# Performance work log

Hardware: AMD Instinct MI355X
Metric: run time of the kernel (lower is better)

The kernel has to match this reference:

```python
import jax, jax.numpy as jnp
import numpy as np

N_NODES = 100000
N_EDGES = 1600000


def setup_inputs() -> dict:
    key = jax.random.key(0)
    k1, k2, k3, k4 = jax.random.split(key, 4)
    x = jax.random.normal(k1, (N_NODES, 16), dtype=jnp.float32)
    edge_index = jax.random.randint(k2, (2, N_EDGES), 0, N_NODES, dtype=jnp.int32)
    # Glorot-ish init for the two GCN layers
    W1 = jax.random.normal(k3, (16, 32), dtype=jnp.float32) * (1.0 / np.sqrt(16))
    b1 = jnp.zeros((32,), dtype=jnp.float32)
    W2 = jax.random.normal(k4, (32, 2), dtype=jnp.float32) * (1.0 / np.sqrt(32))
    b2 = jnp.zeros((2,), dtype=jnp.float32)
    return {"x": x, "edge_index": edge_index, "W1": W1, "b1": b1, "W2": W2, "b2": b2}


def _gcn_conv(x, W, b, src, dst, norm, n_nodes):
    # PyG GCNConv: h = X @ W; aggregate norm * h[src] at dst; add bias.
    h = x @ W                                   # [N, out]
    msg = h[src] * norm[:, None]                # [E+N, out] gather + scale
    out = jax.ops.segment_sum(msg, dst, num_segments=n_nodes)
    return out + b


def reference(x, edge_index, W1, b1, W2, b2):
    n = x.shape[0]
    self_loops = jnp.arange(n, dtype=edge_index.dtype)
    src = jnp.concatenate([edge_index[0], self_loops])  # [E+N]
    dst = jnp.concatenate([edge_index[1], self_loops])
    # Symmetric GCN normalization: deg computed on graph with self-loops
    deg = jax.ops.segment_sum(jnp.ones_like(dst, dtype=x.dtype), dst, num_segments=n)
    dis = jnp.where(deg > 0, jax.lax.rsqrt(deg), 0.0)   # deg^{-1/2}
    norm = dis[src] * dis[dst]                          # [E+N]

    h = jax.nn.relu(_gcn_conv(x, W1, b1, src, dst, norm, n))
    out = _gcn_conv(h, W2, b2, src, dst, norm, n)
    return out
```

## Files before the change

kernel.cpp:

```cpp
#include <hip/hip_runtime.h>
#include <hip/hip_fp16.h>

static constexpr int N  = 100000;
static constexpr int E  = 1600000;
static constexpr int B  = 256;

static constexpr int BC     = 1024;
static constexpr int NBLKC  = 256;
static constexpr int CHUNKC = E / NBLKC;
static constexpr int PERC   = (CHUNKC + BC - 1) / BC;
static constexpr int NBUCK  = (N + 127) / 128;
static constexpr int SLAB   = 3072;
static constexpr int GCS    = 16;


__global__ __launch_bounds__(BC) void kC_scatter(
        const int* __restrict__ src, const int* __restrict__ dst,
        int* __restrict__ gcur, int* __restrict__ gslab) {
    __shared__ int lhist[NBUCK];
    __shared__ int lbase[NBUCK];
    __shared__ int gb[NBUCK];
    __shared__ int wsum[16];
    __shared__ int stage[CHUNKC];

    int t = threadIdx.x, blk = blockIdx.x;
    for (int i = t; i < NBUCK; i += BC) lhist[i] = 0;
    __syncthreads();

    int eb = blk * CHUNKC;
    int ds[PERC], ss[PERC];
#pragma unroll
    for (int k = 0; k < PERC; ++k) {
        int idx = k * BC + t;
        if (idx < CHUNKC) {
            ds[k] = dst[eb + idx];
            ss[k] = src[eb + idx];
            atomicAdd(&lhist[ds[k] >> 7], 1);
        }
    }
    __syncthreads();

    int lane = t & 63, wv = t >> 6;
    int val = (t < NBUCK) ? lhist[t] : 0;
    int inc = val;
#pragma unroll
    for (int off = 1; off < 64; off <<= 1) {
        int u = __shfl_up(inc, off, 64);
        if (lane >= off) inc += u;
    }
    if (lane == 63) wsum[wv] = inc;
    __syncthreads();
    if (wv == 0) {
        int wval = (lane < 16) ? wsum[lane] : 0;
        int winc = wval;
#pragma unroll
        for (int off = 1; off < 16; off <<= 1) {
            int u = __shfl_up(winc, off, 64);
            if (lane >= off) winc += u;
        }
        if (lane < 16) wsum[lane] = winc - wval;
    }
    __syncthreads();
    if (t < NBUCK) lbase[t] = wsum[wv] + inc - val;
    __syncthreads();

    if (t < NBUCK) {
        int h = lhist[t];
        if (h > 0) gb[t] = t * SLAB + atomicAdd(&gcur[t * GCS], h);
        lhist[t] = 0;
    }
    __syncthreads();

#pragma unroll
    for (int k = 0; k < PERC; ++k) {
        int idx = k * BC + t;
        if (idx < CHUNKC) {
            int d = ds[k], b = d >> 7;
            int r = atomicAdd(&lhist[b], 1);
            stage[lbase[b] + r] = ss[k] | ((d & 127) << 17);
        }
    }
    __syncthreads();

    if (t < NBUCK) {
        int len = lhist[t];
        if (len > 0) {
            int s0 = lbase[t];
            int g  = gb[t];
            int cap = (t + 1) * SLAB - g;
            if (cap < 0) cap = 0;
            if (len > cap) len = cap;
            for (int i = 0; i < len; ++i) gslab[g + i] = stage[s0 + i];
        }
    }
}


__global__ void kD1_deg(const int* __restrict__ gcur, const int* __restrict__ gslab,
                        int* __restrict__ rofs, const float4* __restrict__ x4,
                        __half* __restrict__ xpre) {
    __shared__ int c[128];
    __shared__ int wq[2];
    int t = threadIdx.x, b = blockIdx.x;
    if (t < 128) c[t] = 0;
    __syncthreads();

    int ne = min(gcur[b * GCS], SLAB);
    int base = b * SLAB;
    int ne4 = ne & ~3;
    for (int k = 4 * t; k < ne4; k += 4 * B) {
        int4 p4 = *(const int4*)(gslab + base + k);
        atomicAdd(&c[p4.x >> 17], 1);
        atomicAdd(&c[p4.y >> 17], 1);
        atomicAdd(&c[p4.z >> 17], 1);
        atomicAdd(&c[p4.w >> 17], 1);
    }
    if (t < ne - ne4) atomicAdd(&c[gslab[base + ne4 + t] >> 17], 1);
    __syncthreads();

    int lane = t & 63, wv = t >> 6;
    int val = (t < 128) ? c[t] : 0;
    int inc = val;
#pragma unroll
    for (int off = 1; off < 64; off <<= 1) {
        int u = __shfl_up(inc, off, 64);
        if (lane >= off) inc += u;
    }
    if (t == 63) wq[0] = inc;
    __syncthreads();
    if (t < 128) rofs[b * 129 + t] = base + inc - val + ((wv == 1) ? wq[0] : 0);
    if (t == 128) rofs[b * 129 + 128] = base + ne;

    int n = b * 128 + (t >> 1), h = t & 1;
    if (n < N) {
        float d = rsqrtf((float)(c[t >> 1] + 1));
        float4 u0 = x4[(size_t)n * 4 + h * 2];
        float4 u1 = x4[(size_t)n * 4 + h * 2 + 1];
        ushort4 p0, p1;
        p0.x = __half_as_ushort(__float2half(u0.x * d));
        p0.y = __half_as_ushort(__float2half(u0.y * d));
        p0.z = __half_as_ushort(__float2half(u0.z * d));
        p0.w = __half_as_ushort(__float2half(u0.w * d));
        p1.x = __half_as_ushort(__float2half(u1.x * d));
        p1.y = __half_as_ushort(__float2half(u1.y * d));
        p1.z = __half_as_ushort(__float2half(u1.z * d));
        p1.w = __half_as_ushort(__float2half(u1.w * d));
        *(ushort4*)(xpre + (size_t)n * 16 + h * 8)     = p0;
        *(ushort4*)(xpre + (size_t)n * 16 + h * 8 + 4) = p1;
    }
}


__global__ __launch_bounds__(B) void kD2_agg(
        const __half* __restrict__ xpre, const int* __restrict__ gslab,
        const int* __restrict__ rofs, const float* __restrict__ W1,
        const float* __restrict__ b1, const float* __restrict__ W2,
        float2* __restrict__ hpre) {
    __shared__ int st1[SLAB];
    __shared__ int cur[128];
    __shared__ int lofs[129];
    __shared__ float acc[128 * 17];
    __shared__ float sW1[512], sb1[32], sW2[64];
    int t = threadIdx.x, b = blockIdx.x;
    for (int i = t; i < 512; i += B) sW1[i] = W1[i];
    if (t < 32) sb1[t] = b1[t];
    if (t < 64) sW2[t] = W2[t];
    if (t < 128) cur[t] = 0;
    int base = b * SLAB;
    if (t < 129) lofs[t] = rofs[b * 129 + t] - base;
    __syncthreads();

    int ne = lofs[128];
    for (int k = t; k < ne; k += B) {
        int p = gslab[base + k];
        int lo = p >> 17;
        int r = atomicAdd(&cur[lo], 1);
        st1[lofs[lo] + r] = p & 0x1FFFF;
    }
    __syncthreads();

    int nl = t >> 1, h = t & 1;
    int n = b * 128 + nl;
    if (n < N) {
        int rs = lofs[nl], re = lofs[nl + 1];
        float a0, a1, a2, a3, a4, a5, a6, a7;
        {
            int4 w = *(const int4*)(xpre + (size_t)n * 16 + h * 8);
            float2 q0 = __half22float2(*(__half2*)&w.x);
            float2 q1 = __half22float2(*(__half2*)&w.y);
            float2 q2 = __half22float2(*(__half2*)&w.z);
            float2 q3 = __half22float2(*(__half2*)&w.w);
            a0 = q0.x; a1 = q0.y; a2 = q1.x; a3 = q1.y;
            a4 = q2.x; a5 = q2.y; a6 = q3.x; a7 = q3.y;
        }
        auto add8 = [&](int4 w) {
            float2 q0 = __half22float2(*(__half2*)&w.x);
            float2 q1 = __half22float2(*(__half2*)&w.y);
            float2 q2 = __half22float2(*(__half2*)&w.z);
            float2 q3 = __half22float2(*(__half2*)&w.w);
            a0 += q0.x; a1 += q0.y; a2 += q1.x; a3 += q1.y;
            a4 += q2.x; a5 += q2.y; a6 += q3.x; a7 += q3.y;
        };
        int k = rs;
        for (; k + 4 <= re; k += 4) {
            int s0 = st1[k], s1 = st1[k + 1], s2 = st1[k + 2], s3 = st1[k + 3];
            int4 v0 = *(const int4*)(xpre + (size_t)s0 * 16 + h * 8);
            int4 v1 = *(const int4*)(xpre + (size_t)s1 * 16 + h * 8);
            int4 v2 = *(const int4*)(xpre + (size_t)s2 * 16 + h * 8);
            int4 v3 = *(const int4*)(xpre + (size_t)s3 * 16 + h * 8);
            add8(v0); add8(v1); add8(v2); add8(v3);
        }
        for (; k < re; ++k)
            add8(*(const int4*)(xpre + (size_t)st1[k] * 16 + h * 8));
        float* row = acc + nl * 17 + h * 8;
        row[0] = a0; row[1] = a1; row[2] = a2; row[3] = a3;
        row[4] = a4; row[5] = a5; row[6] = a6; row[7] = a7;
    }
    __syncthreads();

    if (t < 128) {
        int n2 = b * 128 + t;
        if (n2 < N) {
            int deg = lofs[t + 1] - lofs[t];
            float d = rsqrtf((float)(deg + 1));
            const float* row = acc + t * 17;
            float xi[16];
#pragma unroll
            for (int k = 0; k < 16; ++k) xi[k] = row[k] * d;
            float o0 = 0.f, o1 = 0.f;
#pragma unroll
            for (int c = 0; c < 32; ++c) {
                float hh = sb1[c];
#pragma unroll
                for (int k = 0; k < 16; ++k) hh = fmaf(xi[k], sW1[k * 32 + c], hh);
                hh = fmaxf(hh, 0.f);
                o0 = fmaf(hh, sW2[c * 2 + 0], o0);
                o1 = fmaf(hh, sW2[c * 2 + 1], o1);
            }
            hpre[n2] = make_float2(d * o0, d * o1);
        }
    }
}


__global__ __launch_bounds__(B) void kF_l2(
        const float2* __restrict__ hpre, const int* __restrict__ gslab,
        const int* __restrict__ rofs, const float* __restrict__ b2,
        float2* __restrict__ out) {
    __shared__ int st1[SLAB];
    __shared__ int cur[128];
    __shared__ int lofs[129];
    int t = threadIdx.x, b = blockIdx.x;
    if (t < 128) cur[t] = 0;
    int base = b * SLAB;
    if (t < 129) lofs[t] = rofs[b * 129 + t] - base;
    __syncthreads();

    int ne = lofs[128];
    for (int k = t; k < ne; k += B) {
        int p = gslab[base + k];
        int lo = p >> 17;
        int r = atomicAdd(&cur[lo], 1);
        st1[lofs[lo] + r] = p & 0x1FFFF;
    }
    __syncthreads();

    int nl = t >> 1, eh = t & 1;
    int n = b * 128 + nl;
    float o0 = 0.f, o1 = 0.f;
    int rs = 0, re = 0;
    if (n < N) {
        rs = lofs[nl]; re = lofs[nl + 1];
        if (eh == 0) {
            float2 self = hpre[n];
            o0 = self.x; o1 = self.y;
        }
        int k = rs + eh;
        for (; k + 6 < re; k += 8) {
            int s0 = st1[k], s1 = st1[k + 2], s2 = st1[k + 4], s3 = st1[k + 6];
            float2 v0 = hpre[s0];
            float2 v1 = hpre[s1];
            float2 v2 = hpre[s2];
            float2 v3 = hpre[s3];
            o0 += (v0.x + v1.x) + (v2.x + v3.x);
            o1 += (v0.y + v1.y) + (v2.y + v3.y);
        }
        for (; k < re; k += 2) {
            float2 v = hpre[st1[k]];
            o0 += v.x; o1 += v.y;
        }
    }
    o0 += __shfl_xor(o0, 1, 64);
    o1 += __shfl_xor(o1, 1, 64);
    if (n < N && eh == 0) {
        float d = rsqrtf((float)(re - rs + 1));
        out[n] = make_float2(fmaf(d, o0, b2[0]), fmaf(d, o1, b2[1]));
    }
}


extern "C" void kernel_launch(void* const* d_in, const int* in_sizes, int n_in,
                              void* d_out, int out_size, void* d_ws, size_t ws_size,
                              hipStream_t stream) {
    const float* x  = (const float*)d_in[0];
    const int*   ei = (const int*)d_in[1];
    const float* W1 = (const float*)d_in[2];
    const float* b1 = (const float*)d_in[3];
    const float* W2 = (const float*)d_in[4];
    const float* b2 = (const float*)d_in[5];

    const int* src = ei;
    const int* dst = ei + E;

    int*    gslab = (int*)d_ws;
    int*    rofs  = gslab + (size_t)NBUCK * SLAB;
    int*    gcur  = rofs + 100880;
    float*  hpre  = (float*)(gcur + 12512);
    __half* xpre  = (__half*)(hpre + 2 * (size_t)N);

    hipMemsetAsync(gcur, 0, NBUCK * GCS * sizeof(int), stream);
    kC_scatter<<<NBLKC, BC, 0, stream>>>(src, dst, gcur, gslab);
    kD1_deg<<<NBUCK, B, 0, stream>>>(gcur, gslab, rofs, (const float4*)x, xpre);
    kD2_agg<<<NBUCK, B, 0, stream>>>(xpre, gslab, rofs, W1, b1, W2, (float2*)hpre);
    kF_l2<<<NBUCK, B, 0, stream>>>((const float2*)hpre, gslab, rofs, b2,
                                   (float2*)d_out);
}
```

Baseline: 128.3 us.

## Fuse all GCN phases into one cooperative kernel with grid syncs

Replaces the memset and four separate kernel launches with a single cooperative kernel of 256 blocks of 1024 threads, using grid.sync between phases and a shared-memory union for the per-phase scratch. Row offsets stay in shared memory across phases instead of a global rofs array. Layer 1 sorts each bucket's edges once and writes the sorted slab back, so layer 2 can load it directly. The aggregation loops now split edges across 4 or 8 lanes per node and reduce with shuffles. This removes launch gaps and a memset, but the bucket phases run at 4 rounds per block and occupancy is limited to one large block per CU.

```diff
diff --git a/kernel.cpp b/kernel.cpp
--- a/kernel.cpp
+++ b/kernel.cpp
@@ -1,300 +1,332 @@
 #include <hip/hip_runtime.h>
 #include <hip/hip_fp16.h>
+#include <hip/hip_cooperative_groups.h>
+
+namespace cg = cooperative_groups;
 
 static constexpr int N  = 100000;
 static constexpr int E  = 1600000;
-static constexpr int B  = 256;
 
 static constexpr int BC     = 1024;
-static constexpr int NBLKC  = 256;
-static constexpr int CHUNKC = E / NBLKC;
+static constexpr int NBLK   = 256;
+static constexpr int CHUNKC = E / NBLK;
 static constexpr int PERC   = (CHUNKC + BC - 1) / BC;
 static constexpr int NBUCK  = (N + 127) / 128;
 static constexpr int SLAB   = 3072;
 static constexpr int GCS    = 16;
-
-
-__global__ __launch_bounds__(BC) void kC_scatter(
+static constexpr int ROUNDS = (NBUCK + NBLK - 1) / NBLK;
+
+struct PhC {
+    int lhist[NBUCK];
+    int lbase[NBUCK];
+    int gb[NBUCK];
+    int wsum[16];
+    int stage[CHUNKC];
+};
+struct PhD1 {
+    int c[128];
+    int wq[2];
+};
+struct PhD2 {
+    int   st1[SLAB];
+    int   cur[128];
+    float acc[128 * 17];
+    float sW1[512];
+    float sb1[32];
+    float sW2[64];
+};
+struct PhF {
+    int st1[SLAB];
+};
+union Smem {
+    PhC  c;
+    PhD1 d1;
+    PhD2 d2;
+    PhF  f;
+};
+
+__global__ __launch_bounds__(BC, 1) void kFused(
         const int* __restrict__ src, const int* __restrict__ dst,
-        int* __restrict__ gcur, int* __restrict__ gslab) {
-    __shared__ int lhist[NBUCK];
-    __shared__ int lbase[NBUCK];
-    __shared__ int gb[NBUCK];
-    __shared__ int wsum[16];
-    __shared__ int stage[CHUNKC];
-
+        const float4* __restrict__ x4,
+        const float* __restrict__ W1, const float* __restrict__ b1,
+        const float* __restrict__ W2, const float* __restrict__ b2,
+        int* __restrict__ gslab, int* __restrict__ gcur,
+        float2* __restrict__ hpre, __half* __restrict__ xpre,
+        float2* __restrict__ out) {
+    __shared__ Smem sm;
+    __shared__ int lofs[ROUNDS][129];
+    cg::grid_group grid = cg::this_grid();
     int t = threadIdx.x, blk = blockIdx.x;
-    for (int i = t; i < NBUCK; i += BC) lhist[i] = 0;
-    __syncthreads();
-
-    int eb = blk * CHUNKC;
-    int ds[PERC], ss[PERC];
-#pragma unroll
-    for (int k = 0; k < PERC; ++k) {
-        int idx = k * BC + t;
-        if (idx < CHUNKC) {
-            ds[k] = dst[eb + idx];
-            ss[k] = src[eb + idx];
-            atomicAdd(&lhist[ds[k] >> 7], 1);
-        }
-    }
-    __syncthreads();
-
-    int lane = t & 63, wv = t >> 6;
-    int val = (t < NBUCK) ? lhist[t] : 0;
-    int inc = val;
-#pragma unroll
-    for (int off = 1; off < 64; off <<= 1) {
-        int u = __shfl_up(inc, off, 64);
-        if (lane >= off) inc += u;
-    }
-    if (lane == 63) wsum[wv] = inc;
-    __syncthreads();
-    if (wv == 0) {
-        int wval = (lane < 16) ? wsum[lane] : 0;
-        int winc = wval;
-#pragma unroll
-        for (int off = 1; off < 16; off <<= 1) {
-            int u = __shfl_up(winc, off, 64);
-            if (lane >= off) winc += u;
-        }
-        if (lane < 16) wsum[lane] = winc - wval;
-    }
-    __syncthreads();
-    if (t < NBUCK) lbase[t] = wsum[wv] + inc - val;
-    __syncthreads();
-
-    if (t < NBUCK) {
-        int h = lhist[t];
-        if (h > 0) gb[t] = t * SLAB + atomicAdd(&gcur[t * GCS], h);
-        lhist[t] = 0;
-    }
-    __syncthreads();
-
-#pragma unroll
-    for (int k = 0; k < PERC; ++k) {
-        int idx = k * BC + t;
-        if (idx < CHUNKC) {
-            int d = ds[k], b = d >> 7;
-            int r = atomicAdd(&lhist[b], 1);
-            stage[lbase[b] + r] = ss[k] | ((d & 127) << 17);
-        }
-    }
-    __syncthreads();
-
-    if (t < NBUCK) {
-        int len = lhist[t];
-        if (len > 0) {
-            int s0 = lbase[t];
-            int g  = gb[t];
-            int cap = (t + 1) * SLAB - g;
-            if (cap < 0) cap = 0;
-            if (len > cap) len = cap;
-            for (int i = 0; i < len; ++i) gslab[g + i] = stage[s0 + i];
-        }
-    }
-}
-
-
-__global__ void kD1_deg(const int* __restrict__ gcur, const int* __restrict__ gslab,
-                        int* __restrict__ rofs, const float4* __restrict__ x4,
-                        __half* __restrict__ xpre) {
-    __shared__ int c[128];
-    __shared__ int wq[2];
-    int t = threadIdx.x, b = blockIdx.x;
-    if (t < 128) c[t] = 0;
-    __syncthreads();
-
-    int ne = min(gcur[b * GCS], SLAB);
-    int base = b * SLAB;
-    int ne4 = ne & ~3;
-    for (int k = 4 * t; k < ne4; k += 4 * B) {
-        int4 p4 = *(const int4*)(gslab + base + k);
-        atomicAdd(&c[p4.x >> 17], 1);
-        atomicAdd(&c[p4.y >> 17], 1);
-        atomicAdd(&c[p4.z >> 17], 1);
-        atomicAdd(&c[p4.w >> 17], 1);
-    }
-    if (t < ne - ne4) atomicAdd(&c[gslab[base + ne4 + t] >> 17], 1);
-    __syncthreads();
-
-    int lane = t & 63, wv = t >> 6;
-    int val = (t < 128) ? c[t] : 0;
-    int inc = val;
-#pragma unroll
-    for (int off = 1; off < 64; off <<= 1) {
-        int u = __shfl_up(inc, off, 64);
-        if (lane >= off) inc += u;
-    }
-    if (t == 63) wq[0] = inc;
-    __syncthreads();
-    if (t < 128) rofs[b * 129 + t] = base + inc - val + ((wv == 1) ? wq[0] : 0);
-    if (t == 128) rofs[b * 129 + 128] = base + ne;
-
-    int n = b * 128 + (t >> 1), h = t & 1;
-    if (n < N) {
-        float d = rsqrtf((float)(c[t >> 1] + 1));
-        float4 u0 = x4[(size_t)n * 4 + h * 2];
-        float4 u1 = x4[(size_t)n * 4 + h * 2 + 1];
-        ushort4 p0, p1;
-        p0.x = __half_as_ushort(__float2half(u0.x * d));
-        p0.y = __half_as_ushort(__float2half(u0.y * d));
-        p0.z = __half_as_ushort(__float2half(u0.z * d));
-        p0.w = __half_as_ushort(__float2half(u0.w * d));
-        p1.x = __half_as_ushort(__float2half(u1.x * d));
-        p1.y = __half_as_ushort(__float2half(u1.y * d));
-        p1.z = __half_as_ushort(__float2half(u1.z * d));
-        p1.w = __half_as_ushort(__float2half(u1.w * d));
-        *(ushort4*)(xpre + (size_t)n * 16 + h * 8)     = p0;
-        *(ushort4*)(xpre + (size_t)n * 16 + h * 8 + 4) = p1;
-    }
-}
-
-
-__global__ __launch_bounds__(B) void kD2_agg(
-        const __half* __restrict__ xpre, const int* __restrict__ gslab,
-        const int* __restrict__ rofs, const float* __restrict__ W1,
-        const float* __restrict__ b1, const float* __restrict__ W2,
-        float2* __restrict__ hpre) {
-    __shared__ int st1[SLAB];
-    __shared__ int cur[128];
-    __shared__ int lofs[129];
-    __shared__ float acc[128 * 17];
-    __shared__ float sW1[512], sb1[32], sW2[64];
-    int t = threadIdx.x, b = blockIdx.x;
-    for (int i = t; i < 512; i += B) sW1[i] = W1[i];
-    if (t < 32) sb1[t] = b1[t];
-    if (t < 64) sW2[t] = W2[t];
-    if (t < 128) cur[t] = 0;
-    int base = b * SLAB;
-    if (t < 129) lofs[t] = rofs[b * 129 + t] - base;
-    __syncthreads();
-
-    int ne = lofs[128];
-    for (int k = t; k < ne; k += B) {
-        int p = gslab[base + k];
-        int lo = p >> 17;
-        int r = atomicAdd(&cur[lo], 1);
-        st1[lofs[lo] + r] = p & 0x1FFFF;
-    }
-    __syncthreads();
-
-    int nl = t >> 1, h = t & 1;
-    int n = b * 128 + nl;
-    if (n < N) {
-        int rs = lofs[nl], re = lofs[nl + 1];
-        float a0, a1, a2, a3, a4, a5, a6, a7;
-        {
-            int4 w = *(const int4*)(xpre + (size_t)n * 16 + h * 8);
-            float2 q0 = __half22float2(*(__half2*)&w.x);
-            float2 q1 = __half22float2(*(__half2*)&w.y);
-            float2 q2 = __half22float2(*(__half2*)&w.z);
-            float2 q3 = __half22float2(*(__half2*)&w.w);
-            a0 = q0.x; a1 = q0.y; a2 = q1.x; a3 = q1.y;
-            a4 = q2.x; a5 = q2.y; a6 = q3.x; a7 = q3.y;
-        }
-        auto add8 = [&](int4 w) {
-            float2 q0 = __half22float2(*(__half2*)&w.x);
-            float2 q1 = __half22float2(*(__half2*)&w.y);
-            float2 q2 = __half22float2(*(__half2*)&w.z);
-            float2 q3 = __half22float2(*(__half2*)&w.w);
-            a0 += q0.x; a1 += q0.y; a2 += q1.x; a3 += q1.y;
-            a4 += q2.x; a5 += q2.y; a6 += q3.x; a7 += q3.y;
-        };
-        int k = rs;
-        for (; k + 4 <= re; k += 4) {
-            int s0 = st1[k], s1 = st1[k + 1], s2 = st1[k + 2], s3 = st1[k + 3];
-            int4 v0 = *(const int4*)(xpre + (size_t)s0 * 16 + h * 8);
-            int4 v1 = *(const int4*)(xpre + (size_t)s1 * 16 + h * 8);
-            int4 v2 = *(const int4*)(xpre + (size_t)s2 * 16 + h * 8);
-            int4 v3 = *(const int4*)(xpre + (size_t)s3 * 16 + h * 8);
-            add8(v0); add8(v1); add8(v2); add8(v3);
-        }
-        for (; k < re; ++k)
-            add8(*(const int4*)(xpre + (size_t)st1[k] * 16 + h * 8));
-        float* row = acc + nl * 17 + h * 8;
-        row[0] = a0; row[1] = a1; row[2] = a2; row[3] = a3;
-        row[4] = a4; row[5] = a5; row[6] = a6; row[7] = a7;
-    }
-    __syncthreads();
-
-    if (t < 128) {
-        int n2 = b * 128 + t;
-        if (n2 < N) {
-            int deg = lofs[t + 1] - lofs[t];
-            float d = rsqrtf((float)(deg + 1));
-            const float* row = acc + t * 17;
-            float xi[16];
-#pragma unroll
-            for (int k = 0; k < 16; ++k) xi[k] = row[k] * d;
-            float o0 = 0.f, o1 = 0.f;
-#pragma unroll
-            for (int c = 0; c < 32; ++c) {
-                float hh = sb1[c];
-#pragma unroll
-                for (int k = 0; k < 16; ++k) hh = fmaf(xi[k], sW1[k * 32 + c], hh);
-                hh = fmaxf(hh, 0.f);
-                o0 = fmaf(hh, sW2[c * 2 + 0], o0);
-                o1 = fmaf(hh, sW2[c * 2 + 1], o1);
-            }
-            hpre[n2] = make_float2(d * o0, d * o1);
-        }
-    }
-}
-
-
-__global__ __launch_bounds__(B) void kF_l2(
-        const float2* __restrict__ hpre, const int* __restrict__ gslab,
-        const int* __restrict__ rofs, const float* __restrict__ b2,
-        float2* __restrict__ out) {
-    __shared__ int st1[SLAB];
-    __shared__ int cur[128];
-    __shared__ int lofs[129];
-    int t = threadIdx.x, b = blockIdx.x;
-    if (t < 128) cur[t] = 0;
-    int base = b * SLAB;
-    if (t < 129) lofs[t] = rofs[b * 129 + t] - base;
-    __syncthreads();
-
-    int ne = lofs[128];
-    for (int k = t; k < ne; k += B) {
-        int p = gslab[base + k];
-        int lo = p >> 17;
-        int r = atomicAdd(&cur[lo], 1);
-        st1[lofs[lo] + r] = p & 0x1FFFF;
-    }
-    __syncthreads();
-
-    int nl = t >> 1, eh = t & 1;
-    int n = b * 128 + nl;
-    float o0 = 0.f, o1 = 0.f;
-    int rs = 0, re = 0;
-    if (n < N) {
-        rs = lofs[nl]; re = lofs[nl + 1];
-        if (eh == 0) {
-            float2 self = hpre[n];
-            o0 = self.x; o1 = self.y;
-        }
-        int k = rs + eh;
-        for (; k + 6 < re; k += 8) {
-            int s0 = st1[k], s1 = st1[k + 2], s2 = st1[k + 4], s3 = st1[k + 6];
-            float2 v0 = hpre[s0];
-            float2 v1 = hpre[s1];
-            float2 v2 = hpre[s2];
-            float2 v3 = hpre[s3];
-            o0 += (v0.x + v1.x) + (v2.x + v3.x);
-            o1 += (v0.y + v1.y) + (v2.y + v3.y);
-        }
-        for (; k < re; k += 2) {
-            float2 v = hpre[st1[k]];
-            o0 += v.x; o1 += v.y;
-        }
-    }
-    o0 += __shfl_xor(o0, 1, 64);
-    o1 += __shfl_xor(o1, 1, 64);
-    if (n < N && eh == 0) {
-        float d = rsqrtf((float)(re - rs + 1));
-        out[n] = make_float2(fmaf(d, o0, b2[0]), fmaf(d, o1, b2[1]));
+
+    {
+        int i = blk * BC + t;
+        if (i < NBUCK * GCS) gcur[i] = 0;
+    }
+    grid.sync();
+
+    {
+        for (int i = t; i < NBUCK; i += BC) sm.c.lhist[i] = 0;
+        __syncthreads();
+
+        int eb = blk * CHUNKC;
+        int ds[PERC], ss[PERC];
+#pragma unroll
+        for (int k = 0; k < PERC; ++k) {
+            int idx = k * BC + t;
+            if (idx < CHUNKC) {
+                ds[k] = dst[eb + idx];
+                ss[k] = src[eb + idx];
+                atomicAdd(&sm.c.lhist[ds[k] >> 7], 1);
+            }
+        }
+        __syncthreads();
+
+        int lane = t & 63, wv = t >> 6;
+        int val = (t < NBUCK) ? sm.c.lhist[t] : 0;
+        int inc = val;
+#pragma unroll
+        for (int off = 1; off < 64; off <<= 1) {
+            int u = __shfl_up(inc, off, 64);
+            if (lane >= off) inc += u;
+        }
+        if (lane == 63) sm.c.wsum[wv] = inc;
+        __syncthreads();
+        if (wv == 0) {
+            int wval = (lane < 16) ? sm.c.wsum[lane] : 0;
+            int winc = wval;
+#pragma unroll
+            for (int off = 1; off < 16; off <<= 1) {
+                int u = __shfl_up(winc, off, 64);
+                if (lane >= off) winc += u;
+            }
+            if (lane < 16) sm.c.wsum[lane] = winc - wval;
+        }
+        __syncthreads();
+        if (t < NBUCK) sm.c.lbase[t] = sm.c.wsum[wv] + inc - val;
+        __syncthreads();
+
+        if (t < NBUCK) {
+            int h = sm.c.lhist[t];
+            if (h > 0) sm.c.gb[t] = t * SLAB + atomicAdd(&gcur[t * GCS], h);
+            sm.c.lhist[t] = 0;
+        }
+        __syncthreads();
+
+#pragma unroll
+        for (int k = 0; k < PERC; ++k) {
+            int idx = k * BC + t;
+            if (idx < CHUNKC) {
+                int d = ds[k], bk = d >> 7;
+                int r = atomicAdd(&sm.c.lhist[bk], 1);
+                sm.c.stage[sm.c.lbase[bk] + r] = ss[k] | ((d & 127) << 17);
+            }
+        }
+        __syncthreads();
+
+        if (t < NBUCK) {
+            int len = sm.c.lhist[t];
+            if (len > 0) {
+                int s0 = sm.c.lbase[t];
+                int g  = sm.c.gb[t];
+                int cap = (t + 1) * SLAB - g;
+                if (cap < 0) cap = 0;
+                if (len > cap) len = cap;
+                for (int i = 0; i < len; ++i) gslab[g + i] = sm.c.stage[s0 + i];
+            }
+        }
+    }
+    grid.sync();
+
+    for (int rd = 0; rd < ROUNDS; ++rd) {
+        int b = rd * NBLK + blk;
+        bool ok = b < NBUCK;
+        if (t < 128) sm.d1.c[t] = 0;
+        __syncthreads();
+
+        int ne = 0, base = 0;
+        if (ok) {
+            ne = min(gcur[b * GCS], SLAB);
+            base = b * SLAB;
+            int ne4 = ne & ~3;
+            for (int k = 4 * t; k < ne4; k += 4 * BC) {
+                int4 p4 = *(const int4*)(gslab + base + k);
+                atomicAdd(&sm.d1.c[p4.x >> 17], 1);
+                atomicAdd(&sm.d1.c[p4.y >> 17], 1);
+                atomicAdd(&sm.d1.c[p4.z >> 17], 1);
+                atomicAdd(&sm.d1.c[p4.w >> 17], 1);
+            }
+            if (t < ne - ne4) atomicAdd(&sm.d1.c[gslab[base + ne4 + t] >> 17], 1);
+        }
+        __syncthreads();
+
+        int lane = t & 63, wv = t >> 6;
+        int val = (t < 128) ? sm.d1.c[t] : 0;
+        int inc = val;
+#pragma unroll
+        for (int off = 1; off < 64; off <<= 1) {
+            int u = __shfl_up(inc, off, 64);
+            if (lane >= off) inc += u;
+        }
+        if (t == 63) sm.d1.wq[0] = inc;
+        __syncthreads();
+        if (t < 128) lofs[rd][t] = inc - val + ((wv == 1) ? sm.d1.wq[0] : 0);
+        if (t == 128) lofs[rd][128] = ne;
+
+        int n = b * 128 + (t >> 1), h = t & 1;
+        if (ok && t < 256 && n < N) {
+            float dd = rsqrtf((float)(sm.d1.c[t >> 1] + 1));
+            float4 u0 = x4[(size_t)n * 4 + h * 2];
+            float4 u1 = x4[(size_t)n * 4 + h * 2 + 1];
+            ushort4 p0, p1;
+            p0.x = __half_as_ushort(__float2half(u0.x * dd));
+            p0.y = __half_as_ushort(__float2half(u0.y * dd));
+            p0.z = __half_as_ushort(__float2half(u0.z * dd));
+            p0.w = __half_as_ushort(__float2half(u0.w * dd));
+            p1.x = __half_as_ushort(__float2half(u1.x * dd));
+            p1.y = __half_as_ushort(__float2half(u1.y * dd));
+            p1.z = __half_as_ushort(__float2half(u1.z * dd));
+            p1.w = __half_as_ushort(__float2half(u1.w * dd));
+            *(ushort4*)(xpre + (size_t)n * 16 + h * 8)     = p0;
+            *(ushort4*)(xpre + (size_t)n * 16 + h * 8 + 4) = p1;
+        }
+        __syncthreads();
+    }
+    grid.sync();
+
+    for (int i = t; i < 512; i += BC) sm.d2.sW1[i] = W1[i];
+    if (t < 32) sm.d2.sb1[t] = b1[t];
+    if (t < 64) sm.d2.sW2[t] = W2[t];
+
+    for (int rd = 0; rd < ROUNDS; ++rd) {
+        int b = rd * NBLK + blk;
+        bool ok = b < NBUCK;
+        int base = b * SLAB;
+        int ne = lofs[rd][128];
+        if (t < 128) sm.d2.cur[t] = 0;
+        __syncthreads();
+
+        if (ok) {
+            for (int k = t; k < ne; k += BC) {
+                int p = gslab[base + k];
+                int lo = p >> 17;
+                int r = atomicAdd(&sm.d2.cur[lo], 1);
+                sm.d2.st1[lofs[rd][lo] + r] = p & 0x1FFFF;
+            }
+        }
+        __syncthreads();
+
+        if (ok) for (int k = t; k < ne; k += BC) gslab[base + k] = sm.d2.st1[k];
+
+        int h  = t & 1;
+        int e  = (t >> 1) & 3;
+        int nl = t >> 3;
+        int n  = b * 128 + nl;
+        float a0 = 0.f, a1 = 0.f, a2 = 0.f, a3 = 0.f,
+              a4 = 0.f, a5 = 0.f, a6 = 0.f, a7 = 0.f;
+        if (ok && n < N) {
+            int rs = lofs[rd][nl], re = lofs[rd][nl + 1];
+            auto add8 = [&](int4 w) {
+                float2 q0 = __half22float2(*(__half2*)&w.x);
+                float2 q1 = __half22float2(*(__half2*)&w.y);
+                float2 q2 = __half22float2(*(__half2*)&w.z);
+                float2 q3 = __half22float2(*(__half2*)&w.w);
+                a0 += q0.x; a1 += q0.y; a2 += q1.x; a3 += q1.y;
+                a4 += q2.x; a5 += q2.y; a6 += q3.x; a7 += q3.y;
+            };
+            if (e == 0)
+                add8(*(const int4*)(xpre + (size_t)n * 16 + h * 8));
+            int k = rs + e;
+            for (; k + 4 < re; k += 8) {
+                int s0 = sm.d2.st1[k], s1 = sm.d2.st1[k + 4];
+                int4 v0 = *(const int4*)(xpre + (size_t)s0 * 16 + h * 8);
+                int4 v1 = *(const int4*)(xpre + (size_t)s1 * 16 + h * 8);
+                add8(v0); add8(v1);
+            }
+            if (k < re)
+                add8(*(const int4*)(xpre + (size_t)sm.d2.st1[k] * 16 + h * 8));
+        }
+        a0 += __shfl_xor(a0, 2, 64); a1 += __shfl_xor(a1, 2, 64);
+        a2 += __shfl_xor(a2, 2, 64); a3 += __shfl_xor(a3, 2, 64);
+        a4 += __shfl_xor(a4, 2, 64); a5 += __shfl_xor(a5, 2, 64);
+        a6 += __shfl_xor(a6, 2, 64); a7 += __shfl_xor(a7, 2, 64);
+        a0 += __shfl_xor(a0, 4, 64); a1 += __shfl_xor(a1, 4, 64);
+        a2 += __shfl_xor(a2, 4, 64); a3 += __shfl_xor(a3, 4, 64);
+        a4 += __shfl_xor(a4, 4, 64); a5 += __shfl_xor(a5, 4, 64);
+        a6 += __shfl_xor(a6, 4, 64); a7 += __shfl_xor(a7, 4, 64);
+        if (ok && n < N && e == 0) {
+            float* row = sm.d2.acc + nl * 17 + h * 8;
+            row[0] = a0; row[1] = a1; row[2] = a2; row[3] = a3;
+            row[4] = a4; row[5] = a5; row[6] = a6; row[7] = a7;
+        }
+        __syncthreads();
+
+        if (ok && t < 128) {
+            int n2 = b * 128 + t;
+            if (n2 < N) {
+                int deg = lofs[rd][t + 1] - lofs[rd][t];
+                float dd = rsqrtf((float)(deg + 1));
+                const float* row = sm.d2.acc + t * 17;
+                float xi[16];
+#pragma unroll
+                for (int k = 0; k < 16; ++k) xi[k] = row[k] * dd;
+                float o0 = 0.f, o1 = 0.f;
+#pragma unroll
+                for (int c = 0; c < 32; ++c) {
+                    float hh = sm.d2.sb1[c];
+#pragma unroll
+                    for (int k = 0; k < 16; ++k)
+                        hh = fmaf(xi[k], sm.d2.sW1[k * 32 + c], hh);
+                    hh = fmaxf(hh, 0.f);
+                    o0 = fmaf(hh, sm.d2.sW2[c * 2 + 0], o0);
+                    o1 = fmaf(hh, sm.d2.sW2[c * 2 + 1], o1);
+                }
+                hpre[n2] = make_float2(dd * o0, dd * o1);
+            }
+        }
+        __syncthreads();
+    }
+    grid.sync();
+
+    float b20 = b2[0], b21 = b2[1];
+    for (int rd = 0; rd < ROUNDS; ++rd) {
+        int b = rd * NBLK + blk;
+        bool ok = b < NBUCK;
+        int base = b * SLAB;
+        int ne = lofs[rd][128];
+        if (ok) for (int k = t; k < ne; k += BC) sm.f.st1[k] = gslab[base + k];
+        __syncthreads();
+
+        int e8 = t & 7, nl = t >> 3;
+        int n = b * 128 + nl;
+        float o0 = 0.f, o1 = 0.f;
+        int deg = 0;
+        if (ok && n < N) {
+            int rs = lofs[rd][nl], re = lofs[rd][nl + 1];
+            deg = re - rs;
+            if (e8 == 0) {
+                float2 s = hpre[n];
+                o0 = s.x; o1 = s.y;
+            }
+            int k = rs + e8;
+            for (; k + 8 < re; k += 16) {
+                float2 v0 = hpre[sm.f.st1[k]];
+                float2 v1 = hpre[sm.f.st1[k + 8]];
+                o0 += v0.x + v1.x;
+                o1 += v0.y + v1.y;
+            }
+            if (k < re) {
+                float2 v = hpre[sm.f.st1[k]];
+                o0 += v.x; o1 += v.y;
+            }
+        }
+        o0 += __shfl_xor(o0, 1, 64); o1 += __shfl_xor(o1, 1, 64);
+        o0 += __shfl_xor(o0, 2, 64); o1 += __shfl_xor(o1, 2, 64);
+        o0 += __shfl_xor(o0, 4, 64); o1 += __shfl_xor(o1, 4, 64);
+        if (ok && n < N && e8 == 0) {
+            float dd = rsqrtf((float)(deg + 1));
+            out[n] = make_float2(fmaf(dd, o0, b20), fmaf(dd, o1, b21));
+        }
+        __syncthreads();
     }
 }
 
@@ -309,19 +341,20 @@
     const float* W2 = (const float*)d_in[4];
     const float* b2 = (const float*)d_in[5];
 
-    const int* src = ei;
-    const int* dst = ei + E;
+    const int* srcp = ei;
+    const int* dstp = ei + E;
+    const float4* x4p = (const float4*)x;
 
     int*    gslab = (int*)d_ws;
-    int*    rofs  = gslab + (size_t)NBUCK * SLAB;
-    int*    gcur  = rofs + 100880;
-    float*  hpre  = (float*)(gcur + 12512);
-    __half* xpre  = (__half*)(hpre + 2 * (size_t)N);
-
-    hipMemsetAsync(gcur, 0, NBUCK * GCS * sizeof(int), stream);
-    kC_scatter<<<NBLKC, BC, 0, stream>>>(src, dst, gcur, gslab);
-    kD1_deg<<<NBUCK, B, 0, stream>>>(gcur, gslab, rofs, (const float4*)x, xpre);
-    kD2_agg<<<NBUCK, B, 0, stream>>>(xpre, gslab, rofs, W1, b1, W2, (float2*)hpre);
-    kF_l2<<<NBUCK, B, 0, stream>>>((const float2*)hpre, gslab, rofs, b2,
-                                   (float2*)d_out);
+    int*    gcur  = gslab + (size_t)NBUCK * SLAB;
+    float2* hprep = (float2*)(gcur + NBUCK * GCS);
+    __half* xprep = (__half*)((float*)hprep + 2 * (size_t)N);
+    float2* outp  = (float2*)d_out;
+
+    void* args[] = {
+        (void*)&srcp, (void*)&dstp, (void*)&x4p,
+        (void*)&W1, (void*)&b1, (void*)&W2, (void*)&b2,
+        (void*)&gslab, (void*)&gcur, (void*)&hprep, (void*)&xprep, (void*)&outp
+    };
+    hipLaunchCooperativeKernel(kFused, dim3(NBLK), dim3(BC), args, 0, stream);
 }
```

Result: slower. 262.1 us (+104.2%).

## Write sorted CSR back from agg kernel and widen gather blocks to 512

Applied to the files above, without the earlier changes.

kD2_agg now writes its locally sorted neighbor list back to the global slab, so kF_l2 can do a straight vectorized copy into shared memory instead of repeating the atomic-based local sort. Both aggregation kernels move to 512-thread blocks with four lanes per node instead of two, splitting each node's edges across lanes and combining the partial sums with wave shuffles. This aims to raise memory-level parallelism in the gathers and remove redundant sort work. The cost is extra global writes in kD2 and more shuffle reductions.

```diff
diff --git a/kernel.cpp b/kernel.cpp
--- a/kernel.cpp
+++ b/kernel.cpp
@@ -4,6 +4,7 @@
 static constexpr int N  = 100000;
 static constexpr int E  = 1600000;
 static constexpr int B  = 256;
+static constexpr int BG = 512;
 
 static constexpr int BC     = 1024;
 static constexpr int NBLKC  = 256;
@@ -151,8 +152,8 @@
 }
 
 
-__global__ __launch_bounds__(B) void kD2_agg(
-        const __half* __restrict__ xpre, const int* __restrict__ gslab,
+__global__ __launch_bounds__(BG) void kD2_agg(
+        const __half* __restrict__ xpre, int* __restrict__ gslab,
         const int* __restrict__ rofs, const float* __restrict__ W1,
         const float* __restrict__ b1, const float* __restrict__ W2,
         float2* __restrict__ hpre) {
@@ -162,7 +163,7 @@
     __shared__ float acc[128 * 17];
     __shared__ float sW1[512], sb1[32], sW2[64];
     int t = threadIdx.x, b = blockIdx.x;
-    for (int i = t; i < 512; i += B) sW1[i] = W1[i];
+    sW1[t] = W1[t];
     if (t < 32) sb1[t] = b1[t];
     if (t < 64) sW2[t] = W2[t];
     if (t < 128) cur[t] = 0;
@@ -171,7 +172,7 @@
     __syncthreads();
 
     int ne = lofs[128];
-    for (int k = t; k < ne; k += B) {
+    for (int k = t; k < ne; k += BG) {
         int p = gslab[base + k];
         int lo = p >> 17;
         int r = atomicAdd(&cur[lo], 1);
@@ -179,20 +180,17 @@
     }
     __syncthreads();
 
-    int nl = t >> 1, h = t & 1;
+    int ne4 = ne & ~3;
+    for (int k = 4 * t; k < ne4; k += 4 * BG)
+        *(int4*)(gslab + base + k) = *(const int4*)(st1 + k);
+    for (int k = ne4 + t; k < ne; k += BG)
+        gslab[base + k] = st1[k];
+
+    int h = t & 1, e = (t >> 1) & 1, nl = t >> 2;
     int n = b * 128 + nl;
+    float a0 = 0.f, a1 = 0.f, a2 = 0.f, a3 = 0.f,
+          a4 = 0.f, a5 = 0.f, a6 = 0.f, a7 = 0.f;
     if (n < N) {
-        int rs = lofs[nl], re = lofs[nl + 1];
-        float a0, a1, a2, a3, a4, a5, a6, a7;
-        {
-            int4 w = *(const int4*)(xpre + (size_t)n * 16 + h * 8);
-            float2 q0 = __half22float2(*(__half2*)&w.x);
-            float2 q1 = __half22float2(*(__half2*)&w.y);
-            float2 q2 = __half22float2(*(__half2*)&w.z);
-            float2 q3 = __half22float2(*(__half2*)&w.w);
-            a0 = q0.x; a1 = q0.y; a2 = q1.x; a3 = q1.y;
-            a4 = q2.x; a5 = q2.y; a6 = q3.x; a7 = q3.y;
-        }
         auto add8 = [&](int4 w) {
             float2 q0 = __half22float2(*(__half2*)&w.x);
             float2 q1 = __half22float2(*(__half2*)&w.y);
@@ -201,17 +199,24 @@
             a0 += q0.x; a1 += q0.y; a2 += q1.x; a3 += q1.y;
             a4 += q2.x; a5 += q2.y; a6 += q3.x; a7 += q3.y;
         };
-        int k = rs;
-        for (; k + 4 <= re; k += 4) {
-            int s0 = st1[k], s1 = st1[k + 1], s2 = st1[k + 2], s3 = st1[k + 3];
+        int rs = lofs[nl], re = lofs[nl + 1];
+        if (e == 0)
+            add8(*(const int4*)(xpre + (size_t)n * 16 + h * 8));
+        int k = rs + e;
+        for (; k + 2 < re; k += 4) {
+            int s0 = st1[k], s1 = st1[k + 2];
             int4 v0 = *(const int4*)(xpre + (size_t)s0 * 16 + h * 8);
             int4 v1 = *(const int4*)(xpre + (size_t)s1 * 16 + h * 8);
-            int4 v2 = *(const int4*)(xpre + (size_t)s2 * 16 + h * 8);
-            int4 v3 = *(const int4*)(xpre + (size_t)s3 * 16 + h * 8);
-            add8(v0); add8(v1); add8(v2); add8(v3);
-        }
-        for (; k < re; ++k)
+            add8(v0); add8(v1);
+        }
+        if (k < re)
             add8(*(const int4*)(xpre + (size_t)st1[k] * 16 + h * 8));
+    }
+    a0 += __shfl_xor(a0, 2, 64); a1 += __shfl_xor(a1, 2, 64);
+    a2 += __shfl_xor(a2, 2, 64); a3 += __shfl_xor(a3, 2, 64);
+    a4 += __shfl_xor(a4, 2, 64); a5 += __shfl_xor(a5, 2, 64);
+    a6 += __shfl_xor(a6, 2, 64); a7 += __shfl_xor(a7, 2, 64);
+    if (n < N && e == 0) {
         float* row = acc + nl * 17 + h * 8;
         row[0] = a0; row[1] = a1; row[2] = a2; row[3] = a3;
         row[4] = a4; row[5] = a5; row[6] = a6; row[7] = a7;
@@ -243,57 +248,52 @@
 }
 
 
-__global__ __launch_bounds__(B) void kF_l2(
+__global__ __launch_bounds__(BG) void kF_l2(
         const float2* __restrict__ hpre, const int* __restrict__ gslab,
         const int* __restrict__ rofs, const float* __restrict__ b2,
         float2* __restrict__ out) {
     __shared__ int st1[SLAB];
-    __shared__ int cur[128];
     __shared__ int lofs[129];
     int t = threadIdx.x, b = blockIdx.x;
-    if (t < 128) cur[t] = 0;
     int base = b * SLAB;
     if (t < 129) lofs[t] = rofs[b * 129 + t] - base;
     __syncthreads();
 
     int ne = lofs[128];
-    for (int k = t; k < ne; k += B) {
-        int p = gslab[base + k];
-        int lo = p >> 17;
-        int r = atomicAdd(&cur[lo], 1);
-        st1[lofs[lo] + r] = p & 0x1FFFF;
-    }
-    __syncthreads();
-
-    int nl = t >> 1, eh = t & 1;
+    int ne4 = ne & ~3;
+    for (int k = 4 * t; k < ne4; k += 4 * BG)
+        *(int4*)(st1 + k) = *(const int4*)(gslab + base + k);
+    for (int k = ne4 + t; k < ne; k += BG)
+        st1[k] = gslab[base + k];
+    __syncthreads();
+
+    int e = t & 3, nl = t >> 2;
     int n = b * 128 + nl;
     float o0 = 0.f, o1 = 0.f;
-    int rs = 0, re = 0;
+    int deg = 0;
     if (n < N) {
-        rs = lofs[nl]; re = lofs[nl + 1];
-        if (eh == 0) {
+        int rs = lofs[nl], re = lofs[nl + 1];
+        deg = re - rs;
+        if (e == 0) {
             float2 self = hpre[n];
             o0 = self.x; o1 = self.y;
         }
-        int k = rs + eh;
-        for (; k + 6 < re; k += 8) {
-            int s0 = st1[k], s1 = st1[k + 2], s2 = st1[k + 4], s3 = st1[k + 6];
-            float2 v0 = hpre[s0];
-            float2 v1 = hpre[s1];
-            float2 v2 = hpre[s2];
-            float2 v3 = hpre[s3];
-            o0 += (v0.x + v1.x) + (v2.x + v3.x);
-            o1 += (v0.y + v1.y) + (v2.y + v3.y);
-        }
-        for (; k < re; k += 2) {
+        int k = rs + e;
+        for (; k + 4 < re; k += 8) {
+            float2 v0 = hpre[st1[k]];
+            float2 v1 = hpre[st1[k + 4]];
+            o0 += v0.x + v1.x;
+            o1 += v0.y + v1.y;
+        }
+        if (k < re) {
             float2 v = hpre[st1[k]];
             o0 += v.x; o1 += v.y;
         }
     }
-    o0 += __shfl_xor(o0, 1, 64);
-    o1 += __shfl_xor(o1, 1, 64);
-    if (n < N && eh == 0) {
-        float d = rsqrtf((float)(re - rs + 1));
+    o0 += __shfl_xor(o0, 1, 64); o1 += __shfl_xor(o1, 1, 64);
+    o0 += __shfl_xor(o0, 2, 64); o1 += __shfl_xor(o1, 2, 64);
+    if (n < N && e == 0) {
+        float d = rsqrtf((float)(deg + 1));
         out[n] = make_float2(fmaf(d, o0, b2[0]), fmaf(d, o1, b2[1]));
     }
 }
@@ -321,7 +321,7 @@
     hipMemsetAsync(gcur, 0, NBUCK * GCS * sizeof(int), stream);
     kC_scatter<<<NBLKC, BC, 0, stream>>>(src, dst, gcur, gslab);
     kD1_deg<<<NBUCK, B, 0, stream>>>(gcur, gslab, rofs, (const float4*)x, xpre);
-    kD2_agg<<<NBUCK, B, 0, stream>>>(xpre, gslab, rofs, W1, b1, W2, (float2*)hpre);
-    kF_l2<<<NBUCK, B, 0, stream>>>((const float2*)hpre, gslab, rofs, b2,
-                                   (float2*)d_out);
-}
+    kD2_agg<<<NBUCK, BG, 0, stream>>>(xpre, gslab, rofs, W1, b1, W2, (float2*)hpre);
+    kF_l2<<<NBUCK, BG, 0, stream>>>((const float2*)hpre, gslab, rofs, b2,
+                                    (float2*)d_out);
+}
```

Measured after the change: 128.9 us. Within noise of the previous version (+0.5%).
